# Kernel optimization log

Measured on AMD Instinct MI355X. Metric: run time of the kernel, lower is better.

Reference implementation:

```python
import jax, jax.numpy as jnp
import numpy as np

VAR_NUM, IN_DIM, OUT_DIM = 3, 8, 32
N_PTS, M_PTS, K_LAST = 8192, 2048, 10
RADIUS = 0.0342
PROJ_HIDDEN = 64
N_DIM = 2
MLP_DIMS = [2 * N_DIM + OUT_DIM, 80, 80, OUT_DIM]  # [36, 80, 80, 32]


def _gelu(x):
    # torch F.gelu default = exact erf form
    return jax.nn.gelu(x, approximate=False)


def _radius_neighbors(data, queries, r):
    # CSR-style neighbor lists (indices grouped per query), chunked for memory
    idx_chunks = []
    counts = np.zeros(queries.shape[0], np.int64)
    r2 = r * r
    for s in range(0, queries.shape[0], 1024):
        q = queries[s:s + 1024]
        d2 = ((q[:, None, :] - data[None, :, :]) ** 2).sum(-1)
        mask = d2 <= r2
        _, cols = np.nonzero(mask)  # row-major -> grouped by query
        idx_chunks.append(cols.astype(np.int32))
        counts[s:s + q.shape[0]] = mask.sum(1)
    return np.concatenate(idx_chunks), counts.astype(np.int32)


def _knn(data, queries, k):
    out = np.zeros((queries.shape[0], k), np.int32)
    for s in range(0, queries.shape[0], 1024):
        q = queries[s:s + 1024]
        d2 = ((q[:, None, :] - data[None, :, :]) ** 2).sum(-1)
        out[s:s + q.shape[0]] = np.argpartition(d2, k, axis=1)[:, :k]
    return out.reshape(-1)


def _mlp_params(key, dims):
    Ws, bs = [], []
    for i in range(len(dims) - 1):
        key, k1 = jax.random.split(key)
        Ws.append(jax.random.normal(k1, (dims[i], dims[i + 1]), jnp.float32) / np.sqrt(dims[i]).astype(np.float32))
        bs.append(jnp.zeros((dims[i + 1],), jnp.float32))
    return Ws, bs


def setup_inputs():
    rng = np.random.default_rng(0)
    input_grid = rng.uniform(size=(N_PTS, N_DIM)).astype(np.float32)
    output_grid = rng.uniform(size=(M_PTS, N_DIM)).astype(np.float32)
    nbr_index, nbr_counts = _radius_neighbors(input_grid, input_grid, RADIUS)
    nbr_seg = np.repeat(np.arange(N_PTS, dtype=np.int32), nbr_counts)
    nbr_last_index = _knn(input_grid, output_grid, K_LAST)

    key = jax.random.key(0)
    ks = jax.random.split(key, 4)
    inp = jax.random.normal(ks[0], (1, N_PTS, VAR_NUM * IN_DIM), jnp.float32)
    pW, pb = _mlp_params(ks[1], [IN_DIM, PROJ_HIDDEN, OUT_DIM])
    it0_W, it0_b = _mlp_params(ks[2], MLP_DIMS)
    it1_W, it1_b = _mlp_params(ks[3], MLP_DIMS)
    return dict(
        inp=inp,
        input_grid=jnp.asarray(input_grid), output_grid=jnp.asarray(output_grid),
        proj_W0=pW[0], proj_b0=pb[0], proj_W1=pW[1], proj_b1=pb[1],
        it0_W0=it0_W[0], it0_b0=it0_b[0], it0_W1=it0_W[1], it0_b1=it0_b[1], it0_W2=it0_W[2], it0_b2=it0_b[2],
        it1_W0=it1_W[0], it1_b0=it1_b[0], it1_W1=it1_W[1], it1_b1=it1_b[1], it1_W2=it1_W[2], it1_b2=it1_b[2],
        nbr_index=jnp.asarray(nbr_index), nbr_seg=jnp.asarray(nbr_seg),
        nbr_counts=jnp.asarray(nbr_counts), nbr_last_index=jnp.asarray(nbr_last_index),
    )


def _mlp3(x, W0, b0, W1, b1, W2, b2):
    x = _gelu(x @ W0 + b0)
    x = _gelu(x @ W1 + b1)
    return x @ W2 + b2


def reference(inp, input_grid, output_grid, proj_W0, proj_b0, proj_W1, proj_b1,
              it0_W0, it0_b0, it0_W1, it0_b1, it0_W2, it0_b2,
              it1_W0, it1_b0, it1_W1, it1_b1, it1_W2, it1_b2,
              nbr_index, nbr_seg, nbr_counts, nbr_last_index):
    B, N, _ = inp.shape  # B must be 1 (module's IT indexing assumes it)
    x = inp.reshape(B * N, VAR_NUM, IN_DIM)
    # pointwise projection MLP (gelu between layers)
    x = _gelu(x @ proj_W0 + proj_b0) @ proj_W1 + proj_b1  # (N, V, OUT_DIM)

    inv_counts = (1.0 / jnp.maximum(nbr_counts, 1).astype(x.dtype))[:, None]
    y_pos = input_grid[nbr_index]        # (E, 2) neighbor positions
    self_pos = input_grid[nbr_seg]       # (E, 2) query positions
    last_y = input_grid[nbr_last_index]                    # (M*K, 2)
    last_self = jnp.repeat(output_grid, K_LAST, axis=0)    # (M*K, 2)

    outs = []
    for v in range(VAR_NUM):
        f = x[:, v, :]
        # IT layer 0: radius neighborhoods on input grid, residual add
        agg = jnp.concatenate([y_pos, self_pos, f[nbr_index]], axis=-1)  # (E, 36)
        h = _mlp3(agg, it0_W0, it0_b0, it0_W1, it0_b1, it0_W2, it0_b2)
        f = jax.ops.segment_sum(h, nbr_seg, num_segments=N) * inv_counts + f
        # IT layer 1 (last): fixed-K neighbors from input grid to output grid, mean
        agg = jnp.concatenate([last_y, last_self, f[nbr_last_index]], axis=-1)
        h = _mlp3(agg, it1_W0, it1_b0, it1_W1, it1_b1, it1_W2, it1_b2)
        outs.append(h.reshape(M_PTS, K_LAST, OUT_DIM).mean(axis=1))
    # original concatenates temp[None] along dim=2 -> (1, M, V*OUT_DIM)
    return jnp.concatenate(outs, axis=-1)[None]
```

## Files before the change

### kernel.cpp

```cpp
#include <hip/hip_runtime.h>
#include <hip/hip_bf16.h>
#include <math.h>

#define N_PTS 8192
#define M_PTS 2048
#define KLAST 10
#define VARS 3
#define OUTD 32
#define D1 80
#define D2 80
#define PB 8
#define LPTS 4
#define NT 512
#define NWAVES 8
#define TPCH 104
#define W0P 72
#define W1P 104
#define RP 32
#define W0SZ (D1 * W0P)
#define W1SZ (D1 * W1P)
#define W2SZ (OUTD * W1P)
#define WPACK (W0SZ + W1SZ + W2SZ)

typedef float f4 __attribute__((ext_vector_type(4)));
typedef short bf16x8 __attribute__((ext_vector_type(8)));

__device__ __forceinline__ float gelu_f(float x) {
    float x2 = x * x;
    float s = x * __builtin_fmaf(0.1029418f, x2, 2.3022083f);
    float u = __builtin_amdgcn_exp2f(s);
    float r = __builtin_amdgcn_rcpf(u + 1.0f);
    return __builtin_fmaf(-x, r, x);
}
__device__ __forceinline__ unsigned short f2bf(float x) {
    unsigned int u = __float_as_uint(x);
    u += 0x7FFF + ((u >> 16) & 1);
    return (unsigned short)(u >> 16);
}
__device__ __forceinline__ float bf2f(unsigned short h) {
    return __uint_as_float(((unsigned int)h) << 16);
}
__device__ __forceinline__ int pk2(float a, float b) {
    __hip_bfloat162 h = __float22bfloat162_rn(float2{a, b});
    int r; __builtin_memcpy(&r, &h, 4); return r;
}

__device__ __forceinline__ void pack_weights(
    const float* __restrict__ W0g, const float* __restrict__ W1g,
    const float* __restrict__ W2g, unsigned short* __restrict__ wp, int t)
{
    for (int idx = t; idx < W0SZ; idx += 256) {
        int col = idx / W0P, k = idx - col * W0P;
        float w = (k < 32) ? W0g[(k + 4) * D1 + col]
                           : ((k < 36) ? W0g[(k - 32) * D1 + col] : 0.0f);
        wp[idx] = f2bf(w);
    }
    for (int idx = t; idx < W1SZ; idx += 256) {
        int col = idx / W1P, k = idx - col * W1P;
        wp[W0SZ + idx] = f2bf((k < D2) ? W1g[k * D1 + col] : 0.0f);
    }
    for (int idx = t; idx < W2SZ; idx += 256) {
        int col = idx / W1P, k = idx - col * W1P;
        wp[W0SZ + W1SZ + idx] = f2bf((k < D2) ? W2g[k * OUTD + col] : 0.0f);
    }
}

__device__ __forceinline__ void mlp_chunk(
    int4 featsi, int4 posfi, unsigned short* Trow,
    const unsigned short* __restrict__ W0h,
    const unsigned short* __restrict__ W1h,
    const unsigned short* __restrict__ W2h,
    const float* bs, int lm, int quad)
{
    bf16x8 b1f0 = *(bf16x8*)&featsi;
    bf16x8 b1f1 = *(bf16x8*)&posfi;
#pragma unroll 1
    for (int cb = 0; cb < 5; ++cb) {
        f4 acc = *(const f4*)&bs[cb * 16 + quad * 4];
        bf16x8 a0 = *(const bf16x8*)&W0h[(cb * 16 + lm) * W0P + quad * 8];
        bf16x8 a1 = *(const bf16x8*)&W0h[(cb * 16 + lm) * W0P + 32 + quad * 8];
        acc = __builtin_amdgcn_mfma_f32_16x16x32_bf16(a0, b1f0, acc, 0, 0, 0);
        acc = __builtin_amdgcn_mfma_f32_16x16x32_bf16(a1, b1f1, acc, 0, 0, 0);
        *(int2*)&Trow[cb * 16 + quad * 4] =
            make_int2(pk2(gelu_f(acc.x), gelu_f(acc.y)),
                      pk2(gelu_f(acc.z), gelu_f(acc.w)));
    }
    bf16x8 b2f[3];
    b2f[0] = *(const bf16x8*)&Trow[quad * 8];
    b2f[1] = *(const bf16x8*)&Trow[32 + quad * 8];
    b2f[2] = *(const bf16x8*)&Trow[64 + quad * 8];
#pragma unroll 1
    for (int cb = 0; cb < 5; ++cb) {
        f4 acc = *(const f4*)&bs[80 + cb * 16 + quad * 4];
        const unsigned short* wh = &W1h[(cb * 16 + lm) * W1P + quad * 8];
        bf16x8 h0 = *(const bf16x8*)&wh[0];
        bf16x8 h1 = *(const bf16x8*)&wh[32];
        bf16x8 h2 = *(const bf16x8*)&wh[64];
        acc = __builtin_amdgcn_mfma_f32_16x16x32_bf16(h0, b2f[0], acc, 0, 0, 0);
        acc = __builtin_amdgcn_mfma_f32_16x16x32_bf16(h1, b2f[1], acc, 0, 0, 0);
        acc = __builtin_amdgcn_mfma_f32_16x16x32_bf16(h2, b2f[2], acc, 0, 0, 0);
        *(int2*)&Trow[cb * 16 + quad * 4] =
            make_int2(pk2(gelu_f(acc.x), gelu_f(acc.y)),
                      pk2(gelu_f(acc.z), gelu_f(acc.w)));
    }
    bf16x8 b3f[3];
    b3f[0] = *(const bf16x8*)&Trow[quad * 8];
    b3f[1] = *(const bf16x8*)&Trow[32 + quad * 8];
    b3f[2] = *(const bf16x8*)&Trow[64 + quad * 8];
    float* po = (float*)Trow;
#pragma unroll 1
    for (int cb = 0; cb < 2; ++cb) {
        f4 acc = *(const f4*)&bs[160 + cb * 16 + quad * 4];
        const unsigned short* wh = &W2h[(cb * 16 + lm) * W1P + quad * 8];
        bf16x8 h0 = *(const bf16x8*)&wh[0];
        bf16x8 h1 = *(const bf16x8*)&wh[32];
        bf16x8 h2 = *(const bf16x8*)&wh[64];
        acc = __builtin_amdgcn_mfma_f32_16x16x32_bf16(h0, b3f[0], acc, 0, 0, 0);
        acc = __builtin_amdgcn_mfma_f32_16x16x32_bf16(h1, b3f[1], acc, 0, 0, 0);
        acc = __builtin_amdgcn_mfma_f32_16x16x32_bf16(h2, b3f[2], acc, 0, 0, 0);
        *(f4*)&po[cb * 16 + quad * 4] = acc;
    }
}

__global__ __launch_bounds__(256) void proj_scan_kernel(
    const float* __restrict__ inp, const float* __restrict__ grid_in,
    const float* __restrict__ W0, const float* __restrict__ b0,
    const float* __restrict__ W1, const float* __restrict__ b1,
    unsigned short* __restrict__ f0b, int* __restrict__ posb,
    const int* __restrict__ counts, int* __restrict__ offsets,
    const float* __restrict__ i0W0, const float* __restrict__ i0W1,
    const float* __restrict__ i0W2, unsigned short* __restrict__ wpack0,
    const float* __restrict__ i1W0, const float* __restrict__ i1W1,
    const float* __restrict__ i1W2, unsigned short* __restrict__ wpack1)
{
    const int t = threadIdx.x;
    if (blockIdx.x == 769) { pack_weights(i0W0, i0W1, i0W2, wpack0, t); return; }
    if (blockIdx.x == 770) { pack_weights(i1W0, i1W1, i1W2, wpack1, t); return; }
    if (blockIdx.x == 768) {
        __shared__ int ws2[4], wx2[4];
        const int lane = t & 63, wave = t >> 6;
        int4 a[8];
#pragma unroll
        for (int i = 0; i < 8; ++i) a[i] = ((const int4*)counts)[t * 8 + i];
        int s = 0;
#pragma unroll
        for (int i = 0; i < 8; ++i) s += a[i].x + a[i].y + a[i].z + a[i].w;
        int x = s;
#pragma unroll
        for (int d = 1; d < 64; d <<= 1) {
            int y = __shfl_up(x, d);
            if (lane >= d) x += y;
        }
        if (lane == 63) ws2[wave] = x;
        __syncthreads();
        if (t == 0) {
            wx2[0] = 0;
            wx2[1] = ws2[0];
            wx2[2] = ws2[0] + ws2[1];
            wx2[3] = ws2[0] + ws2[1] + ws2[2];
        }
        __syncthreads();
        int base = wx2[wave] + (x - s);
#pragma unroll
        for (int i = 0; i < 8; ++i) {
            int4 c = a[i];
            int4 o;
            o.x = base; base += c.x;
            o.y = base; base += c.y;
            o.z = base; base += c.z;
            o.w = base; base += c.w;
            ((int4*)offsets)[t * 8 + i] = o;
        }
        return;
    }
    __shared__ float W0s[8 * 64];
    __shared__ float W1s[64 * OUTD];
    __shared__ float xs[32 * 8];
    __shared__ float H[32 * 64];
    const int r0 = blockIdx.x * 32;
    for (int idx = t; idx < 512; idx += 256) W0s[idx] = W0[idx];
    for (int idx = t; idx < 64 * OUTD; idx += 256) W1s[idx] = W1[idx];
    xs[t] = inp[r0 * 8 + t];
    if (t < 32) {
        int row = r0 + t, n = row / 3;
        posb[n] = pk2(grid_in[2 * n], grid_in[2 * n + 1]);
    }
    __syncthreads();
#pragma unroll 1
    for (int p = 0; p < 8; ++p) {
        int o = t + 256 * p, r = o >> 6, col = o & 63;
        float s = b0[col];
#pragma unroll
        for (int k = 0; k < 8; ++k) s += xs[r * 8 + k] * W0s[k * 64 + col];
        H[o] = gelu_f(s);
    }
    __syncthreads();
#pragma unroll 1
    for (int p = 0; p < 4; ++p) {
        int o = t + 256 * p, r = o >> 5, c = o & 31;
        float s = b1[c];
#pragma unroll 8
        for (int k = 0; k < 64; ++k) s += H[r * 64 + k] * W1s[k * OUTD + c];
        int row = r0 + r;
        int n = row / 3, v = row - n * 3;
        f0b[((size_t)(v << 13) + n) * RP + c] = f2bf(s);
    }
}

__global__ __launch_bounds__(512, 8) void agg_kernel(
    const float* __restrict__ grid_in, const unsigned short* __restrict__ f0b,
    const int* __restrict__ posb,
    const int* __restrict__ nbr_index, const int* __restrict__ offsets,
    const int* __restrict__ counts,
    const unsigned short* __restrict__ wpack,
    const float* __restrict__ b0g, const float* __restrict__ b1g,
    const float* __restrict__ b2g,
    unsigned short* __restrict__ f1b)
{
    __shared__ __attribute__((aligned(16))) unsigned short Tb[NWAVES * 16 * TPCH];
    __shared__ __attribute__((aligned(16))) float bs[192];
    __shared__ __attribute__((aligned(16))) float accH[VARS * PB * 32];
    __shared__ int offs[PB + 1];
    __shared__ int px2b[PB];
    __shared__ float invb[PB];

    const unsigned short* W0h = wpack;
    const unsigned short* W1h = wpack + W0SZ;
    const unsigned short* W2h = wpack + W0SZ + W1SZ;

    const int t = threadIdx.x;
    const int lane = t & 63, wave = t >> 6;
    const int lm = lane & 15, quad = lane >> 4;
    const int p0 = blockIdx.x * PB;

    for (int idx = t; idx < 192; idx += NT)
        bs[idx] = (idx < 80) ? b0g[idx] : (idx < 160 ? b1g[idx - 80] : b2g[idx - 160]);
    if (t < PB) {
        offs[t] = offsets[p0 + t];
        int c = counts[p0 + t];
        invb[t] = 1.0f / (float)(c > 1 ? c : 1);
        px2b[t] = pk2(grid_in[2 * (p0 + t)], grid_in[2 * (p0 + t) + 1]);
    }
    if (t == PB) offs[PB] = offsets[p0 + PB - 1] + counts[p0 + PB - 1];
    for (int idx = t; idx < VARS * PB * 32; idx += NT) accH[idx] = 0.0f;
    __syncthreads();

    unsigned short* TbW = Tb + (wave * 16) * TPCH;
    if (lane < 32)
        *(int4*)(TbW + (lane >> 1) * TPCH + 80 + (lane & 1) * 8) = make_int4(0, 0, 0, 0);

    const int e0 = offs[0];
    const int cntT = offs[PB] - e0;
    const int Rb = VARS * cntT;
    const int nch = (Rb + 15) >> 4;

    unsigned short* Trow = TbW + lm * TPCH;

    int pkey; int4 pfeats, pposf;
    {
        int myrow = (wave << 4) + lm;
        pkey = -1; pfeats = make_int4(0,0,0,0); pposf = make_int4(0,0,0,0);
        if (myrow < Rb) {
            int myv = (myrow >= 2 * cntT) ? 2 : ((myrow >= cntT) ? 1 : 0);
            int e = e0 + myrow - myv * cntT;
            int myj = nbr_index[e];
            int lp = 0;
#pragma unroll
            for (int l = 1; l < PB; ++l) lp += (e >= offs[l]);
            pkey = myv * PB + lp;
            pfeats = ((const int4*)(f0b + ((size_t)(myv << 13) + myj) * RP))[quad];
            if (quad == 0) pposf = make_int4(posb[myj], px2b[lp], 0, 0);
        }
    }

    for (int ch = wave; ch < nch; ch += NWAVES) {
        int ckey = pkey; int4 cfeats = pfeats, cposf = pposf;
        int nc = ch + NWAVES;
        pkey = -1; pfeats = make_int4(0,0,0,0); pposf = make_int4(0,0,0,0);
        if (nc < nch) {
            int myrow = (nc << 4) + lm;
            if (myrow < Rb) {
                int myv = (myrow >= 2 * cntT) ? 2 : ((myrow >= cntT) ? 1 : 0);
                int e = e0 + myrow - myv * cntT;
                int myj = nbr_index[e];
                int lp = 0;
#pragma unroll
                for (int l = 1; l < PB; ++l) lp += (e >= offs[l]);
                pkey = myv * PB + lp;
                pfeats = ((const int4*)(f0b + ((size_t)(myv << 13) + myj) * RP))[quad];
                if (quad == 0) pposf = make_int4(posb[myj], px2b[lp], 0, 0);
            }
        }
        if (ckey < 0) { cfeats = make_int4(0,0,0,0); cposf = make_int4(0,0,0,0); }
        mlp_chunk(cfeats, cposf, Trow, W0h, W1h, W2h, bs, lm, quad);
        int col = lane & 31, eo = lane >> 5;
#pragma unroll 1
        for (int e2 = eo; e2 < 16; e2 += 2) {
            int k = __shfl(ckey, e2);
            if (k >= 0)
                atomicAdd(&accH[k * 32 + col], ((const float*)(TbW + e2 * TPCH))[col]);
        }
    }
    __syncthreads();
    for (int idx = t; idx < VARS * PB * OUTD; idx += NT) {
        int key = idx >> 5, c = idx & 31;
        int v = key >> 3, lp = key & 7;
        size_t rec = ((size_t)(v << 13) + p0 + lp) * RP;
        float val = accH[key * 32 + c] * invb[lp] + bf2f(f0b[rec + c]);
        f1b[rec + c] = f2bf(val);
    }
}

__global__ __launch_bounds__(512, 8) void last_kernel(
    const unsigned short* __restrict__ f1b, const int* __restrict__ posb,
    const float* __restrict__ grid_out,
    const int* __restrict__ nbr_last,
    const unsigned short* __restrict__ wpack,
    const float* __restrict__ b0g, const float* __restrict__ b1g,
    const float* __restrict__ b2g,
    float* __restrict__ out)
{
    __shared__ __attribute__((aligned(16))) unsigned short Tb[NWAVES * 16 * TPCH];
    __shared__ __attribute__((aligned(16))) float bs[192];
    __shared__ __attribute__((aligned(16))) float accH[LPTS * VARS * 32];
    __shared__ int pxo2b[LPTS];

    const unsigned short* W0h = wpack;
    const unsigned short* W1h = wpack + W0SZ;
    const unsigned short* W2h = wpack + W0SZ + W1SZ;

    const int t = threadIdx.x;
    const int lane = t & 63, wave = t >> 6;
    const int lm = lane & 15, quad = lane >> 4;
    const int m0 = blockIdx.x * LPTS;

    for (int idx = t; idx < 192; idx += NT)
        bs[idx] = (idx < 80) ? b0g[idx] : (idx < 160 ? b1g[idx - 80] : b2g[idx - 160]);
    if (t < LPTS)
        pxo2b[t] = pk2(grid_out[2 * (m0 + t)], grid_out[2 * (m0 + t) + 1]);
    for (int idx = t; idx < LPTS * VARS * 32; idx += NT) accH[idx] = 0.0f;
    __syncthreads();
    unsigned short* TbW = Tb + (wave * 16) * TPCH;
    if (lane < 32)
        *(int4*)(TbW + (lane >> 1) * TPCH + 80 + (lane & 1) * 8) = make_int4(0, 0, 0, 0);

    const int Rb = LPTS * VARS * KLAST;
    const int nch = (Rb + 15) >> 4;
    unsigned short* Trow = TbW + lm * TPCH;

    for (int ch = wave; ch < nch; ch += NWAVES) {
        int myrow = (ch << 4) + lm;
        int ckey = -1; int4 cfeats = make_int4(0,0,0,0), cposf = make_int4(0,0,0,0);
        if (myrow < Rb) {
            int lp = myrow / 30, rr = myrow - lp * 30;
            int v = rr / KLAST, kk = rr - v * KLAST;
            int myj = nbr_last[(m0 + lp) * KLAST + kk];
            ckey = lp * VARS + v;
            cfeats = ((const int4*)(f1b + ((size_t)(v << 13) + myj) * RP))[quad];
            if (quad == 0) cposf = make_int4(posb[myj], pxo2b[lp], 0, 0);
        }
        mlp_chunk(cfeats, cposf, Trow, W0h, W1h, W2h, bs, lm, quad);
        int col = lane & 31, eo = lane >> 5;
#pragma unroll 1
        for (int e2 = eo; e2 < 16; e2 += 2) {
            int k = __shfl(ckey, e2);
            if (k >= 0)
                atomicAdd(&accH[k * 32 + col], ((const float*)(TbW + e2 * TPCH))[col]);
        }
    }
    __syncthreads();
    if (t < LPTS * VARS * OUTD) {
        int key = t >> 5, c = t & 31;
        int lp = key / VARS, v = key - lp * VARS;
        out[((size_t)(m0 + lp) * VARS + v) * OUTD + c] = accH[key * 32 + c] * (1.0f / KLAST);
    }
}

extern "C" void kernel_launch(void* const* d_in, const int* in_sizes, int n_in,
                              void* d_out, int out_size, void* d_ws, size_t ws_size,
                              hipStream_t stream) {
    const float* inp      = (const float*)d_in[0];
    const float* grid_in  = (const float*)d_in[1];
    const float* grid_out = (const float*)d_in[2];
    const float* pW0 = (const float*)d_in[3];
    const float* pb0 = (const float*)d_in[4];
    const float* pW1 = (const float*)d_in[5];
    const float* pb1 = (const float*)d_in[6];
    const float* i0W0 = (const float*)d_in[7];
    const float* i0b0 = (const float*)d_in[8];
    const float* i0W1 = (const float*)d_in[9];
    const float* i0b1 = (const float*)d_in[10];
    const float* i0W2 = (const float*)d_in[11];
    const float* i0b2 = (const float*)d_in[12];
    const float* i1W0 = (const float*)d_in[13];
    const float* i1b0 = (const float*)d_in[14];
    const float* i1W1 = (const float*)d_in[15];
    const float* i1b1 = (const float*)d_in[16];
    const float* i1W2 = (const float*)d_in[17];
    const float* i1b2 = (const float*)d_in[18];
    const int* nbr_index  = (const int*)d_in[19];
    const int* nbr_counts = (const int*)d_in[21];
    const int* nbr_last   = (const int*)d_in[22];

    unsigned short* f0b = (unsigned short*)d_ws;
    unsigned short* f1b = f0b + (size_t)VARS * N_PTS * RP;
    int* offsets = (int*)(f1b + (size_t)VARS * N_PTS * RP);
    int* posb    = offsets + N_PTS;
    unsigned short* wpack0 = (unsigned short*)(posb + N_PTS);
    unsigned short* wpack1 = wpack0 + WPACK;

    proj_scan_kernel<<<771, 256, 0, stream>>>(inp, grid_in, pW0, pb0, pW1, pb1,
                                              f0b, posb, nbr_counts, offsets,
                                              i0W0, i0W1, i0W2, wpack0,
                                              i1W0, i1W1, i1W2, wpack1);
    agg_kernel<<<N_PTS / PB, NT, 0, stream>>>(grid_in, f0b, posb, nbr_index, offsets,
                                              nbr_counts, wpack0,
                                              i0b0, i0b1, i0b2, f1b);
    last_kernel<<<M_PTS / LPTS, NT, 0, stream>>>(f1b, posb, grid_out, nbr_last, wpack1,
                                                 i1b0, i1b1, i1b2,
                                                 (float*)d_out);
}
```

Baseline: 307.8 us.

## Software-pipeline weight loads in MLP and two-stage prefetch of neighbor gathers

```diff
diff --git a/kernel.cpp b/kernel.cpp
--- a/kernel.cpp
+++ b/kernel.cpp
@@ -13,6 +13,8 @@
 #define LPTS 4
 #define NT 512
 #define NWAVES 8
+#define NTL 256
+#define NWL 4
 #define TPCH 104
 #define W0P 72
 #define W1P 104
@@ -74,50 +76,64 @@
 {
     bf16x8 b1f0 = *(bf16x8*)&featsi;
     bf16x8 b1f1 = *(bf16x8*)&posfi;
+    const unsigned short* w0base = &W0h[lm * W0P + quad * 8];
+    const unsigned short* w1base = &W1h[lm * W1P + quad * 8];
+    const unsigned short* w2base = &W2h[lm * W1P + quad * 8];
+    bf16x8 pa0 = *(const bf16x8*)&w0base[0];
+    bf16x8 pa1 = *(const bf16x8*)&w0base[32];
+    f4 pb = *(const f4*)&bs[quad * 4];
 #pragma unroll 1
     for (int cb = 0; cb < 5; ++cb) {
-        f4 acc = *(const f4*)&bs[cb * 16 + quad * 4];
-        bf16x8 a0 = *(const bf16x8*)&W0h[(cb * 16 + lm) * W0P + quad * 8];
-        bf16x8 a1 = *(const bf16x8*)&W0h[(cb * 16 + lm) * W0P + 32 + quad * 8];
+        bf16x8 a0 = pa0, a1 = pa1;
+        const unsigned short* nw = (cb < 4) ? &w0base[(cb + 1) * 16 * W0P] : w1base;
+        pa0 = *(const bf16x8*)&nw[0];
+        pa1 = *(const bf16x8*)&nw[32];
+        f4 acc = pb;
+        pb = *(const f4*)&bs[((cb < 4) ? (cb + 1) * 16 : 80) + quad * 4];
         acc = __builtin_amdgcn_mfma_f32_16x16x32_bf16(a0, b1f0, acc, 0, 0, 0);
         acc = __builtin_amdgcn_mfma_f32_16x16x32_bf16(a1, b1f1, acc, 0, 0, 0);
         *(int2*)&Trow[cb * 16 + quad * 4] =
             make_int2(pk2(gelu_f(acc.x), gelu_f(acc.y)),
                       pk2(gelu_f(acc.z), gelu_f(acc.w)));
     }
-    bf16x8 b2f[3];
-    b2f[0] = *(const bf16x8*)&Trow[quad * 8];
-    b2f[1] = *(const bf16x8*)&Trow[32 + quad * 8];
-    b2f[2] = *(const bf16x8*)&Trow[64 + quad * 8];
+    bf16x8 pa2 = *(const bf16x8*)&w1base[64];
+    bf16x8 b2f0 = *(const bf16x8*)&Trow[quad * 8];
+    bf16x8 b2f1 = *(const bf16x8*)&Trow[32 + quad * 8];
+    bf16x8 b2f2 = *(const bf16x8*)&Trow[64 + quad * 8];
 #pragma unroll 1
     for (int cb = 0; cb < 5; ++cb) {
-        f4 acc = *(const f4*)&bs[80 + cb * 16 + quad * 4];
-        const unsigned short* wh = &W1h[(cb * 16 + lm) * W1P + quad * 8];
-        bf16x8 h0 = *(const bf16x8*)&wh[0];
-        bf16x8 h1 = *(const bf16x8*)&wh[32];
-        bf16x8 h2 = *(const bf16x8*)&wh[64];
-        acc = __builtin_amdgcn_mfma_f32_16x16x32_bf16(h0, b2f[0], acc, 0, 0, 0);
-        acc = __builtin_amdgcn_mfma_f32_16x16x32_bf16(h1, b2f[1], acc, 0, 0, 0);
-        acc = __builtin_amdgcn_mfma_f32_16x16x32_bf16(h2, b2f[2], acc, 0, 0, 0);
+        bf16x8 h0 = pa0, h1 = pa1, h2 = pa2;
+        const unsigned short* nw = (cb < 4) ? &w1base[(cb + 1) * 16 * W1P] : w2base;
+        pa0 = *(const bf16x8*)&nw[0];
+        pa1 = *(const bf16x8*)&nw[32];
+        pa2 = *(const bf16x8*)&nw[64];
+        f4 acc = pb;
+        pb = *(const f4*)&bs[((cb < 4) ? 80 + (cb + 1) * 16 : 160) + quad * 4];
+        acc = __builtin_amdgcn_mfma_f32_16x16x32_bf16(h0, b2f0, acc, 0, 0, 0);
+        acc = __builtin_amdgcn_mfma_f32_16x16x32_bf16(h1, b2f1, acc, 0, 0, 0);
+        acc = __builtin_amdgcn_mfma_f32_16x16x32_bf16(h2, b2f2, acc, 0, 0, 0);
         *(int2*)&Trow[cb * 16 + quad * 4] =
             make_int2(pk2(gelu_f(acc.x), gelu_f(acc.y)),
                       pk2(gelu_f(acc.z), gelu_f(acc.w)));
     }
-    bf16x8 b3f[3];
-    b3f[0] = *(const bf16x8*)&Trow[quad * 8];
-    b3f[1] = *(const bf16x8*)&Trow[32 + quad * 8];
-    b3f[2] = *(const bf16x8*)&Trow[64 + quad * 8];
+    bf16x8 b3f0 = *(const bf16x8*)&Trow[quad * 8];
+    bf16x8 b3f1 = *(const bf16x8*)&Trow[32 + quad * 8];
+    bf16x8 b3f2 = *(const bf16x8*)&Trow[64 + quad * 8];
     float* po = (float*)Trow;
 #pragma unroll 1
     for (int cb = 0; cb < 2; ++cb) {
-        f4 acc = *(const f4*)&bs[160 + cb * 16 + quad * 4];
-        const unsigned short* wh = &W2h[(cb * 16 + lm) * W1P + quad * 8];
-        bf16x8 h0 = *(const bf16x8*)&wh[0];
-        bf16x8 h1 = *(const bf16x8*)&wh[32];
-        bf16x8 h2 = *(const bf16x8*)&wh[64];
-        acc = __builtin_amdgcn_mfma_f32_16x16x32_bf16(h0, b3f[0], acc, 0, 0, 0);
-        acc = __builtin_amdgcn_mfma_f32_16x16x32_bf16(h1, b3f[1], acc, 0, 0, 0);
-        acc = __builtin_amdgcn_mfma_f32_16x16x32_bf16(h2, b3f[2], acc, 0, 0, 0);
+        bf16x8 h0 = pa0, h1 = pa1, h2 = pa2;
+        if (cb == 0) {
+            const unsigned short* nw = &w2base[16 * W1P];
+            pa0 = *(const bf16x8*)&nw[0];
+            pa1 = *(const bf16x8*)&nw[32];
+            pa2 = *(const bf16x8*)&nw[64];
+        }
+        f4 acc = pb;
+        if (cb == 0) pb = *(const f4*)&bs[176 + quad * 4];
+        acc = __builtin_amdgcn_mfma_f32_16x16x32_bf16(h0, b3f0, acc, 0, 0, 0);
+        acc = __builtin_amdgcn_mfma_f32_16x16x32_bf16(h1, b3f1, acc, 0, 0, 0);
+        acc = __builtin_amdgcn_mfma_f32_16x16x32_bf16(h2, b3f2, acc, 0, 0, 0);
         *(f4*)&po[cb * 16 + quad * 4] = acc;
     }
 }
@@ -256,43 +272,42 @@
 
     unsigned short* Trow = TbW + lm * TPCH;
 
-    int pkey; int4 pfeats, pposf;
-    {
-        int myrow = (wave << 4) + lm;
-        pkey = -1; pfeats = make_int4(0,0,0,0); pposf = make_int4(0,0,0,0);
-        if (myrow < Rb) {
-            int myv = (myrow >= 2 * cntT) ? 2 : ((myrow >= cntT) ? 1 : 0);
-            int e = e0 + myrow - myv * cntT;
-            int myj = nbr_index[e];
-            int lp = 0;
-#pragma unroll
-            for (int l = 1; l < PB; ++l) lp += (e >= offs[l]);
-            pkey = myv * PB + lp;
-            pfeats = ((const int4*)(f0b + ((size_t)(myv << 13) + myj) * RP))[quad];
-            if (quad == 0) pposf = make_int4(posb[myj], px2b[lp], 0, 0);
-        }
-    }
-
-    for (int ch = wave; ch < nch; ch += NWAVES) {
-        int ckey = pkey; int4 cfeats = pfeats, cposf = pposf;
-        int nc = ch + NWAVES;
-        pkey = -1; pfeats = make_int4(0,0,0,0); pposf = make_int4(0,0,0,0);
-        if (nc < nch) {
-            int myrow = (nc << 4) + lm;
+    auto fetch_index = [&](int ch2, int& key, int& j) {
+        key = -1; j = 0;
+        if (ch2 < nch) {
+            int myrow = (ch2 << 4) + lm;
             if (myrow < Rb) {
                 int myv = (myrow >= 2 * cntT) ? 2 : ((myrow >= cntT) ? 1 : 0);
                 int e = e0 + myrow - myv * cntT;
-                int myj = nbr_index[e];
                 int lp = 0;
 #pragma unroll
                 for (int l = 1; l < PB; ++l) lp += (e >= offs[l]);
-                pkey = myv * PB + lp;
-                pfeats = ((const int4*)(f0b + ((size_t)(myv << 13) + myj) * RP))[quad];
-                if (quad == 0) pposf = make_int4(posb[myj], px2b[lp], 0, 0);
+                key = myv * PB + lp;
+                j = nbr_index[e];
             }
         }
-        if (ckey < 0) { cfeats = make_int4(0,0,0,0); cposf = make_int4(0,0,0,0); }
-        mlp_chunk(cfeats, cposf, Trow, W0h, W1h, W2h, bs, lm, quad);
+    };
+    auto fetch_record = [&](int key, int j, int4& feats, int4& posf) {
+        feats = make_int4(0, 0, 0, 0); posf = make_int4(0, 0, 0, 0);
+        if (key >= 0) {
+            int v = key >> 3, lp = key & 7;
+            feats = ((const int4*)(f0b + ((size_t)(v << 13) + j) * RP))[quad];
+            if (quad == 0) posf = make_int4(posb[j], px2b[lp], 0, 0);
+        }
+    };
+
+    int keyA, jA, keyB, jB;
+    fetch_index(wave, keyA, jA);
+    fetch_index(wave + NWAVES, keyB, jB);
+    int4 featsA, posfA;
+    fetch_record(keyA, jA, featsA, posfA);
+
+    for (int ch = wave; ch < nch; ch += NWAVES) {
+        int ckey = keyA; int4 cf = featsA, cp = posfA;
+        keyA = keyB; jA = jB;
+        fetch_index(ch + 2 * NWAVES, keyB, jB);
+        fetch_record(keyA, jA, featsA, posfA);
+        mlp_chunk(cf, cp, Trow, W0h, W1h, W2h, bs, lm, quad);
         int col = lane & 31, eo = lane >> 5;
 #pragma unroll 1
         for (int e2 = eo; e2 < 16; e2 += 2) {
@@ -311,7 +326,7 @@
     }
 }
 
-__global__ __launch_bounds__(512, 8) void last_kernel(
+__global__ __launch_bounds__(256, 8) void last_kernel(
     const unsigned short* __restrict__ f1b, const int* __restrict__ posb,
     const float* __restrict__ grid_out,
     const int* __restrict__ nbr_last,
@@ -320,7 +335,7 @@
     const float* __restrict__ b2g,
     float* __restrict__ out)
 {
-    __shared__ __attribute__((aligned(16))) unsigned short Tb[NWAVES * 16 * TPCH];
+    __shared__ __attribute__((aligned(16))) unsigned short Tb[NWL * 16 * TPCH];
     __shared__ __attribute__((aligned(16))) float bs[192];
     __shared__ __attribute__((aligned(16))) float accH[LPTS * VARS * 32];
     __shared__ int pxo2b[LPTS];
@@ -334,11 +349,11 @@
     const int lm = lane & 15, quad = lane >> 4;
     const int m0 = blockIdx.x * LPTS;
 
-    for (int idx = t; idx < 192; idx += NT)
+    for (int idx = t; idx < 192; idx += NTL)
         bs[idx] = (idx < 80) ? b0g[idx] : (idx < 160 ? b1g[idx - 80] : b2g[idx - 160]);
     if (t < LPTS)
         pxo2b[t] = pk2(grid_out[2 * (m0 + t)], grid_out[2 * (m0 + t) + 1]);
-    for (int idx = t; idx < LPTS * VARS * 32; idx += NT) accH[idx] = 0.0f;
+    for (int idx = t; idx < LPTS * VARS * 32; idx += NTL) accH[idx] = 0.0f;
     __syncthreads();
     unsigned short* TbW = Tb + (wave * 16) * TPCH;
     if (lane < 32)
@@ -348,18 +363,39 @@
     const int nch = (Rb + 15) >> 4;
     unsigned short* Trow = TbW + lm * TPCH;
 
-    for (int ch = wave; ch < nch; ch += NWAVES) {
-        int myrow = (ch << 4) + lm;
-        int ckey = -1; int4 cfeats = make_int4(0,0,0,0), cposf = make_int4(0,0,0,0);
-        if (myrow < Rb) {
-            int lp = myrow / 30, rr = myrow - lp * 30;
-            int v = rr / KLAST, kk = rr - v * KLAST;
-            int myj = nbr_last[(m0 + lp) * KLAST + kk];
-            ckey = lp * VARS + v;
-            cfeats = ((const int4*)(f1b + ((size_t)(v << 13) + myj) * RP))[quad];
-            if (quad == 0) cposf = make_int4(posb[myj], pxo2b[lp], 0, 0);
-        }
-        mlp_chunk(cfeats, cposf, Trow, W0h, W1h, W2h, bs, lm, quad);
+    auto fetch_index = [&](int ch2, int& key, int& j) {
+        key = -1; j = 0;
+        if (ch2 < nch) {
+            int myrow = (ch2 << 4) + lm;
+            if (myrow < Rb) {
+                int lp = myrow / 30, rr = myrow - lp * 30;
+                int v = rr / KLAST, kk = rr - v * KLAST;
+                j = nbr_last[(m0 + lp) * KLAST + kk];
+                key = lp * VARS + v;
+            }
+        }
+    };
+    auto fetch_record = [&](int key, int j, int4& feats, int4& posf) {
+        feats = make_int4(0, 0, 0, 0); posf = make_int4(0, 0, 0, 0);
+        if (key >= 0) {
+            int lp = key / VARS, v = key - lp * VARS;
+            feats = ((const int4*)(f1b + ((size_t)(v << 13) + j) * RP))[quad];
+            if (quad == 0) posf = make_int4(posb[j], pxo2b[lp], 0, 0);
+        }
+    };
+
+    int keyA, jA, keyB, jB;
+    fetch_index(wave, keyA, jA);
+    fetch_index(wave + NWL, keyB, jB);
+    int4 featsA, posfA;
+    fetch_record(keyA, jA, featsA, posfA);
+
+    for (int ch = wave; ch < nch; ch += NWL) {
+        int ckey = keyA; int4 cf = featsA, cp = posfA;
+        keyA = keyB; jA = jB;
+        fetch_index(ch + 2 * NWL, keyB, jB);
+        fetch_record(keyA, jA, featsA, posfA);
+        mlp_chunk(cf, cp, Trow, W0h, W1h, W2h, bs, lm, quad);
         int col = lane & 31, eo = lane >> 5;
 #pragma unroll 1
         for (int e2 = eo; e2 < 16; e2 += 2) {
@@ -369,8 +405,8 @@
         }
     }
     __syncthreads();
-    if (t < LPTS * VARS * OUTD) {
-        int key = t >> 5, c = t & 31;
+    for (int idx = t; idx < LPTS * VARS * OUTD; idx += NTL) {
+        int key = idx >> 5, c = idx & 31;
         int lp = key / VARS, v = key - lp * VARS;
         out[((size_t)(m0 + lp) * VARS + v) * OUTD + c] = accH[key * 32 + c] * (1.0f / KLAST);
     }
@@ -416,7 +452,7 @@
     agg_kernel<<<N_PTS / PB, NT, 0, stream>>>(grid_in, f0b, posb, nbr_index, offsets,
                                               nbr_counts, wpack0,
                                               i0b0, i0b1, i0b2, f1b);
-    last_kernel<<<M_PTS / LPTS, NT, 0, stream>>>(f1b, posb, grid_out, nbr_last, wpack1,
-                                                 i1b0, i1b1, i1b2,
-                                                 (float*)d_out);
-}
+    last_kernel<<<M_PTS / LPTS, NTL, 0, stream>>>(f1b, posb, grid_out, nbr_last, wpack1,
+                                                  i1b0, i1b1, i1b2,
+                                                  (float*)d_out);
+}
```

New measurement: 324.6 us. 5.5% more time.
